# Kernel optimization log

Measured on AMD Instinct MI355X. Metric: run time of the kernel, lower is better.

The kernel has to match this reference:

```python
import jax, jax.numpy as jnp
import numpy as np

N_ENT = 200000   # n_entities
N_NODES = 20000  # nodes in subgraph
N_EDGES = 320000 # avg degree 16
R = 40           # n_relations
B = 34           # num_bases (hard-coded in module)
D_IN = 128       # emb_dim_init
D_HID = 128      # hidden_dim
D_OUT = 128      # out_dim


def setup_inputs() -> dict:
    key = jax.random.key(0)
    ks = jax.random.split(key, 14)
    s = 0.05
    return {
        "node_index": jax.random.randint(ks[0], (N_NODES,), 0, N_ENT),
        "edge_index": jax.random.randint(ks[1], (2, N_EDGES), 0, N_NODES),
        "edge_type": jax.random.randint(ks[2], (N_EDGES,), 0, R),
        "node_frequency": jax.random.normal(ks[3], (N_NODES,), jnp.float32),
        "node_emb": jax.random.normal(ks[4], (N_ENT, D_IN), jnp.float32),
        "comp0": jax.random.normal(ks[5], (R, B), jnp.float32) * s,
        "bases0": jax.random.normal(ks[6], (B, D_IN, D_HID), jnp.float32) * s,
        "root0": jax.random.normal(ks[7], (D_IN, D_HID), jnp.float32) * s,
        "bias0": jnp.zeros((D_HID,), jnp.float32),
        "comp1": jax.random.normal(ks[8], (R, B), jnp.float32) * s,
        "bases1": jax.random.normal(ks[9], (B, D_HID, D_OUT), jnp.float32) * s,
        "root1": jax.random.normal(ks[10], (D_HID, D_OUT), jnp.float32) * s,
        "bias1": jnp.zeros((D_OUT,), jnp.float32),
    }


def _rgcn_conv(x, src, dst, etype, comp, bases, root, bias):
    """Basis-decomposed RGCNConv (PyG semantics: per-relation mean aggregation
    over incoming edges, plus root transform and bias)."""
    n = x.shape[0]
    # relation weights from basis decomposition: [R, in, out]
    W = jnp.einsum('rb,bio->rio', comp, bases)
    # transform all nodes by every relation weight: [R, N, out]
    h_all = jnp.einsum('ni,rio->rno', x, W)
    # gather per-edge message x[src] @ W[edge_type]: [E, out]
    msg = h_all[etype, src]
    # mean-aggregate per (dst node, relation) segment
    seg = dst * R + etype
    sums = jax.ops.segment_sum(msg, seg, num_segments=n * R)  # [N*R, out]
    cnt = jax.ops.segment_sum(jnp.ones((msg.shape[0],), x.dtype), seg,
                              num_segments=n * R)
    mean = sums / jnp.maximum(cnt, 1.0)[:, None]
    agg = mean.reshape(n, R, -1).sum(axis=1)  # sum over relations: [N, out]
    return agg + x @ root + bias


def reference(node_index, edge_index, edge_type, node_frequency, node_emb,
              comp0, bases0, root0, bias0, comp1, bases1, root1, bias1):
    # node_frequency is accepted but unused (matches original forward).
    x = node_emb[node_index]                      # [N, D_IN]
    src, dst = edge_index[0], edge_index[1]
    x = _rgcn_conv(x, src, dst, edge_type, comp0, bases0, root0, bias0)
    x = _rgcn_conv(x, src, dst, edge_type, comp1, bases1, root1, bias1)
    return x
```

## Files before the change

kernel.cpp:

```cpp
#include <hip/hip_runtime.h>

#define N_NODES  20000
#define N_EDGES  320000
#define R_REL    40
#define N_BASES  34
#define DIM      128
#define EB       128
#define P_PAD    (N_EDGES + R_REL * EB)
#define ROOT_PAD ((N_NODES + EB - 1) / EB * EB)
#define P2_MAX   (P_PAD + ROOT_PAD)
#define NE2      (N_EDGES + N_NODES)
#define NSLOT    (R_REL + 1)
#define NBLK     (P2_MAX / EB)
#define PADW     (NSLOT * EB)

#define INIT_B   ((N_NODES * R_REL + 255) / 256)
#define GATH_B   (N_NODES * 16 / 256)
#define WT_B     (2 * NSLOT * 16)

typedef unsigned int uint;
typedef unsigned short ushort;
typedef __attribute__((ext_vector_type(8))) short short8;
typedef __attribute__((ext_vector_type(4))) float f32x4;

__device__ __forceinline__ ushort f2bf(float f) {
    uint u = __float_as_uint(f);
    return (ushort)((u + 0x7FFFu + ((u >> 16) & 1u)) >> 16);
}
__device__ __forceinline__ uint pk2bf(float a, float b) {
    return (uint)f2bf(a) | ((uint)f2bf(b) << 16);
}

__global__ void prep_kernel(int* __restrict__ c_cnt, int* __restrict__ meta_cur2_deg,
                            const float* __restrict__ emb, const int* __restrict__ idx,
                            ushort* __restrict__ xb,
                            const float* __restrict__ comp0, const float* __restrict__ bases0,
                            const float* __restrict__ root0,
                            const float* __restrict__ comp1, const float* __restrict__ bases1,
                            const float* __restrict__ root1,
                            ushort* __restrict__ Wt) {
    int b = blockIdx.x;
    int t = threadIdx.x;
    if (b < INIT_B) {
        int i = b * 256 + t;
        if (i < N_NODES * R_REL) c_cnt[i] = 0;
        if (i < 256 + 2 * N_NODES) meta_cur2_deg[i] = 0;
    } else if (b < INIT_B + GATH_B) {
        int g = (b - INIT_B) * 256 + t;
        int n = g >> 4, v = g & 15;
        const float4* s = (const float4*)(emb + (size_t)idx[n] * DIM + v * 8);
        float4 a = s[0], bb = s[1];
        uint4 o;
        o.x = pk2bf(a.x, a.y);  o.y = pk2bf(a.z, a.w);
        o.z = pk2bf(bb.x, bb.y); o.w = pk2bf(bb.z, bb.w);
        *(uint4*)(xb + (size_t)n * DIM + v * 8) = o;
    } else {
        __shared__ float tile[32][33];
        __shared__ float scomp[N_BASES];
        int wb = b - INIT_B - GATH_B;
        int layer = (wb >= NSLOT * 16) ? 1 : 0;
        int bb2 = wb - layer * NSLOT * 16;
        const float* comp  = layer ? comp1  : comp0;
        const float* bases = layer ? bases1 : bases0;
        const float* root  = layer ? root1  : root0;
        int slot = bb2 >> 4;
        int tb   = bb2 & 15;
        int k0 = (tb >> 2) * 32, n0 = (tb & 3) * 32;
        int tr = t >> 5, tc = t & 31;
        if (slot < R_REL) {
            if (t < N_BASES) scomp[t] = comp[slot * N_BASES + t];
            __syncthreads();
            #pragma unroll
            for (int i = 0; i < 4; ++i) {
                int kk = tr + 8 * i;
                float acc = 0.f;
                #pragma unroll
                for (int bs = 0; bs < N_BASES; ++bs)
                    acc += scomp[bs] * bases[((size_t)bs * DIM + k0 + kk) * DIM + n0 + tc];
                tile[kk][tc] = acc;
            }
        } else {
            #pragma unroll
            for (int i = 0; i < 4; ++i) {
                int kk = tr + 8 * i;
                tile[kk][tc] = root[(size_t)(k0 + kk) * DIM + n0 + tc];
            }
        }
        __syncthreads();
        size_t obase = ((size_t)layer * NSLOT + slot) * DIM * DIM;
        #pragma unroll
        for (int i = 0; i < 4; ++i) {
            int rr = tr + 8 * i;
            Wt[obase + (size_t)(n0 + rr) * DIM + k0 + tc] = f2bf(tile[tc][rr]);
        }
    }
}

__global__ void count_kernel(const int* __restrict__ ei, const int* __restrict__ et,
                             int* __restrict__ c, int* __restrict__ h,
                             int* __restrict__ deg) {
    __shared__ int hloc[R_REL];
    int t = threadIdx.x;
    if (t < R_REL) hloc[t] = 0;
    __syncthreads();
    int e = blockIdx.x * blockDim.x + t;
    if (e < N_EDGES) {
        int dst = ei[N_EDGES + e];
        int r   = et[e];
        atomicAdd(&c[dst * R_REL + r], 1);
        atomicAdd(&deg[dst], 1);
        atomicAdd(&hloc[r], 1);
    }
    __syncthreads();
    if (t < R_REL && hloc[t]) atomicAdd(&h[t], hloc[t]);
}

__global__ void scans_kernel(const int* __restrict__ deg, const int* __restrict__ h,
                             int* __restrict__ ptr, int* __restrict__ off,
                             int* __restrict__ brel) {
    __shared__ int part[1024];
    __shared__ int soff[R_REL + 2];
    const int CHn = (N_NODES + 1023) / 1024;
    int t = threadIdx.x;
    int s = 0;
    for (int i = 0; i < CHn; ++i) {
        int idx = t * CHn + i;
        if (idx < N_NODES) s += deg[idx] + 1;
    }
    part[t] = s;
    __syncthreads();
    for (int d = 1; d < 1024; d <<= 1) {
        int v = (t >= d) ? part[t - d] : 0;
        __syncthreads();
        part[t] += v;
        __syncthreads();
    }
    int base = (t > 0) ? part[t - 1] : 0;
    for (int i = 0; i < CHn; ++i) {
        int idx = t * CHn + i;
        if (idx < N_NODES) { ptr[idx] = base; base += deg[idx] + 1; }
    }
    if (t == 0) {
        ptr[N_NODES] = NE2;
        int acc = 0;
        soff[0] = 0; off[0] = 0;
        for (int r = 0; r < R_REL; ++r) {
            acc += ((h[r] + EB - 1) / EB) * EB;
            soff[r + 1] = acc; off[r + 1] = acc;
        }
        soff[R_REL + 1] = acc + ROOT_PAD;
        off[R_REL + 1]  = acc + ROOT_PAD;
    }
    __syncthreads();
    for (int i = t; i < NBLK; i += 1024) {
        int e0 = i * EB;
        int r = -1;
        if (e0 < soff[R_REL + 1]) {
            r = 0;
            while (e0 >= soff[r + 1]) ++r;
        }
        brel[i] = r;
    }
}

__global__ void place_kernel(const int* __restrict__ ei, const int* __restrict__ et,
                             const int* __restrict__ off, int* __restrict__ cur,
                             const int* __restrict__ c_cnt, const int* __restrict__ h,
                             const int* __restrict__ ptr, int* __restrict__ cur2,
                             uint4* __restrict__ esrc) {
    __shared__ int hloc[R_REL];
    __shared__ int base[R_REL];
    int t = threadIdx.x;
    if (t < R_REL) hloc[t] = 0;
    __syncthreads();
    int e = blockIdx.x * blockDim.x + t;
    int r = 0, myrank = 0, src = 0, dst = 0;
    bool isEdge = (e < N_EDGES);
    if (isEdge) {
        r = et[e]; src = ei[e]; dst = ei[N_EDGES + e];
        myrank = atomicAdd(&hloc[r], 1);
    }
    __syncthreads();
    if (t < R_REL) base[t] = hloc[t] ? atomicAdd(&cur[t], hloc[t]) : 0;
    __syncthreads();
    if (isEdge) {
        int p = off[r] + base[r] + myrank;
        int q = ptr[dst] + 1 + atomicAdd(&cur2[dst], 1);
        int cnt = c_cnt[dst * R_REL + r];
        float esc = 1.0f / (float)(cnt < 1 ? 1 : cnt);
        esrc[p] = make_uint4((uint)src, (uint)q, __float_as_uint(esc), 0u);
    } else if (e < NE2) {
        int n = e - N_EDGES;
        esrc[off[R_REL] + n] = make_uint4((uint)n, (uint)ptr[n], 0x3f800000u, 0u);
    } else if (e < NE2 + PADW) {
        int i = e - NE2;
        int pr = i >> 7, j = i & (EB - 1);
        int cnt = (pr < R_REL) ? h[pr] : N_NODES;
        int slot = off[pr] + cnt + j;
        if (slot < off[pr + 1])
            esrc[slot] = make_uint4((uint)-1, (uint)-1, 0u, 0u);
    }
}

__launch_bounds__(512)
__global__ void edge_mfma_kernel(const uint4* __restrict__ esrc, const int* __restrict__ brel,
                                 const ushort* __restrict__ xb, const ushort* __restrict__ Wt,
                                 ushort* __restrict__ T) {
    __shared__ __align__(16) ushort Ws[DIM * DIM];
    int r = brel[blockIdx.x];
    if (r < 0) return;
    int t = threadIdx.x;
    int e0 = blockIdx.x * EB;
    int wv = t >> 6;
    int l  = t & 63;
    int lr = l & 15;
    int lk = l >> 4;
    int er = e0 + wv * 16 + lr;
    uint4 es = esrc[er];

    const ushort* Wr = Wt + (size_t)r * DIM * DIM;
    #pragma unroll
    for (int i = 0; i < 4; ++i) {
        int idx = t + 512 * i;
        int row = idx >> 4, slot = idx & 15;
        uint4 v = *(const uint4*)(Wr + row * DIM + slot * 8);
        *(uint4*)(&Ws[row * DIM + ((slot ^ (row & 15)) * 8)]) = v;
    }

    int s0 = (int)es.x, q0 = (int)es.y;
    float esc = __uint_as_float(es.z);
    const ushort* xp = xb + (size_t)(s0 < 0 ? 0 : s0) * DIM;
    short8 xf[4];
    #pragma unroll
    for (int ks = 0; ks < 4; ++ks)
        xf[ks] = *(const short8*)(xp + (ks * 4 + lk) * 8);
    __syncthreads();

    f32x4 acc[8];
    #pragma unroll
    for (int mt = 0; mt < 8; ++mt) acc[mt] = (f32x4){0.f, 0.f, 0.f, 0.f};

    #pragma unroll
    for (int ks = 0; ks < 4; ++ks) {
        #pragma unroll
        for (int mt = 0; mt < 8; ++mt) {
            int row = mt * 16 + lr;
            int slot = (ks * 4 + lk) ^ lr;
            short8 wf = *(const short8*)(&Ws[row * DIM + slot * 8]);
            acc[mt] = __builtin_amdgcn_mfma_f32_16x16x32_bf16(wf, xf[ks], acc[mt], 0, 0, 0);
        }
    }

    if (q0 >= 0) {
        ushort* T0 = T + (size_t)q0 * DIM;
        #pragma unroll
        for (int mt = 0; mt < 8; ++mt) {
            uint2 p0;
            p0.x = pk2bf(acc[mt][0] * esc, acc[mt][1] * esc);
            p0.y = pk2bf(acc[mt][2] * esc, acc[mt][3] * esc);
            *(uint2*)(T0 + mt * 16 + lk * 4) = p0;
        }
    }
}

template<int OUT_BF16>
__global__ void aggregate_kernel(const int* __restrict__ ptr, const ushort* __restrict__ T,
                                 const float* __restrict__ bias, void* __restrict__ yout) {
    int t = threadIdx.x;
    int n = blockIdx.x * 2 + (t >> 6);
    int tt = t & 63;
    int s0 = ptr[n], s1 = ptr[n + 1];
    float a0 = bias[2 * tt], a1 = bias[2 * tt + 1];
    for (int q = s0; q < s1; ++q) {
        uint v = *(const uint*)(T + (size_t)q * DIM + 2 * tt);
        a0 += __uint_as_float(v << 16);
        a1 += __uint_as_float(v & 0xFFFF0000u);
    }
    if (OUT_BF16) {
        ((uint*)yout)[n * 64 + tt] = pk2bf(a0, a1);
    } else {
        ((float2*)yout)[n * 64 + tt] = make_float2(a0, a1);
    }
}

extern "C" void kernel_launch(void* const* d_in, const int* in_sizes, int n_in,
                              void* d_out, int out_size, void* d_ws, size_t ws_size,
                              hipStream_t stream) {
    const int*   node_index = (const int*)d_in[0];
    const int*   edge_index = (const int*)d_in[1];
    const int*   edge_type  = (const int*)d_in[2];
    const float* node_emb   = (const float*)d_in[4];
    const float* comp0  = (const float*)d_in[5];
    const float* bases0 = (const float*)d_in[6];
    const float* root0  = (const float*)d_in[7];
    const float* bias0  = (const float*)d_in[8];
    const float* comp1  = (const float*)d_in[9];
    const float* bases1 = (const float*)d_in[10];
    const float* root1  = (const float*)d_in[11];
    const float* bias1  = (const float*)d_in[12];
    float* out = (float*)d_out;

    char* ws = (char*)d_ws;
    int*    c_cnt  = (int*)   (ws);
    ushort* Wt     = (ushort*)(ws +  3200000);
    ushort* x0b    = (ushort*)(ws +  5886976);
    ushort* y0b    = (ushort*)(ws + 11006976);
    uint4*  esrc   = (uint4*) (ws + 16126976);
    int*    meta   = (int*)   (ws + 21650432);
    int*    cur2   = (int*)   (ws + 21651456);
    int*    deg    = (int*)   (ws + 21731456);
    int*    ptr    = (int*)   (ws + 21811456);
    int*    brel   = (int*)   (ws + 21891712);
    ushort* T      = (ushort*)(ws + 21904000);
    int* off = meta;
    int* h   = meta + 64;
    int* cur = meta + 128;

    prep_kernel<<<INIT_B + GATH_B + WT_B, 256, 0, stream>>>(
        c_cnt, meta, node_emb, node_index, x0b,
        comp0, bases0, root0, comp1, bases1, root1, Wt);
    count_kernel<<<(N_EDGES + 255) / 256, 256, 0, stream>>>(edge_index, edge_type, c_cnt, h, deg);
    scans_kernel<<<1, 1024, 0, stream>>>(deg, h, ptr, off, brel);
    place_kernel<<<(NE2 + PADW + 255) / 256, 256, 0, stream>>>(
        edge_index, edge_type, off, cur, c_cnt, h, ptr, cur2, esrc);

    edge_mfma_kernel<<<NBLK, 512, 0, stream>>>(esrc, brel, x0b, Wt, T);
    aggregate_kernel<1><<<N_NODES / 2, 128, 0, stream>>>(ptr, T, bias0, y0b);

    edge_mfma_kernel<<<NBLK, 512, 0, stream>>>(esrc, brel, y0b,
                                               Wt + (size_t)NSLOT * DIM * DIM, T);
    aggregate_kernel<0><<<N_NODES / 2, 128, 0, stream>>>(ptr, T, bias1, out);
}
```

Baseline: 255.4 us.

## Compute 20 relation weights per block reusing each loaded basis tile

The weight-construction blocks in the prep kernel now each compute 20 relations for one 32x32 tile, and each loaded basis element is reused across all 20 relations. Previously every relation re-read all 34 bases separately. Basis reads drop by about 20x, but the launch shrinks from 1312 weight blocks to 64 and each thread carries 80 accumulators, which lowers parallelism and raises register pressure.

```diff
diff --git a/kernel.cpp b/kernel.cpp
--- a/kernel.cpp
+++ b/kernel.cpp
@@ -16,7 +16,7 @@
 
 #define INIT_B   ((N_NODES * R_REL + 255) / 256)
 #define GATH_B   (N_NODES * 16 / 256)
-#define WT_B     (2 * NSLOT * 16)
+#define WT_B     64
 
 typedef unsigned int uint;
 typedef unsigned short ushort;
@@ -56,42 +56,63 @@
         *(uint4*)(xb + (size_t)n * DIM + v * 8) = o;
     } else {
         __shared__ float tile[32][33];
-        __shared__ float scomp[N_BASES];
+        __shared__ float scomp[20][N_BASES];
         int wb = b - INIT_B - GATH_B;
-        int layer = (wb >= NSLOT * 16) ? 1 : 0;
-        int bb2 = wb - layer * NSLOT * 16;
+        int layer = wb >> 5;
+        int chunk = (wb >> 4) & 1;
+        int tb    = wb & 15;
         const float* comp  = layer ? comp1  : comp0;
         const float* bases = layer ? bases1 : bases0;
         const float* root  = layer ? root1  : root0;
-        int slot = bb2 >> 4;
-        int tb   = bb2 & 15;
         int k0 = (tb >> 2) * 32, n0 = (tb & 3) * 32;
+        int cr0 = chunk * 20;
         int tr = t >> 5, tc = t & 31;
-        if (slot < R_REL) {
-            if (t < N_BASES) scomp[t] = comp[slot * N_BASES + t];
+        for (int i = t; i < 20 * N_BASES; i += 256)
+            scomp[i / N_BASES][i % N_BASES] = comp[(cr0 + i / N_BASES) * N_BASES + i % N_BASES];
+        __syncthreads();
+        float acc[20][4];
+        #pragma unroll
+        for (int r = 0; r < 20; ++r)
+            #pragma unroll
+            for (int i = 0; i < 4; ++i) acc[r][i] = 0.f;
+        for (int bs = 0; bs < N_BASES; ++bs) {
+            float t4[4];
+            #pragma unroll
+            for (int i = 0; i < 4; ++i)
+                t4[i] = bases[((size_t)bs * DIM + k0 + tr + 8 * i) * DIM + n0 + tc];
+            #pragma unroll
+            for (int r = 0; r < 20; ++r) {
+                float cv = scomp[r][bs];
+                #pragma unroll
+                for (int i = 0; i < 4; ++i) acc[r][i] += cv * t4[i];
+            }
+        }
+        size_t lbase = (size_t)layer * NSLOT * DIM * DIM;
+        #pragma unroll 1
+        for (int r = 0; r < 20; ++r) {
             __syncthreads();
             #pragma unroll
+            for (int i = 0; i < 4; ++i) tile[tr + 8 * i][tc] = acc[r][i];
+            __syncthreads();
+            size_t obase = lbase + (size_t)(cr0 + r) * DIM * DIM;
+            #pragma unroll
             for (int i = 0; i < 4; ++i) {
-                int kk = tr + 8 * i;
-                float acc = 0.f;
-                #pragma unroll
-                for (int bs = 0; bs < N_BASES; ++bs)
-                    acc += scomp[bs] * bases[((size_t)bs * DIM + k0 + kk) * DIM + n0 + tc];
-                tile[kk][tc] = acc;
+                int rr = tr + 8 * i;
+                Wt[obase + (size_t)(n0 + rr) * DIM + k0 + tc] = f2bf(tile[tc][rr]);
             }
-        } else {
+        }
+        if (chunk == 1) {
+            __syncthreads();
+            #pragma unroll
+            for (int i = 0; i < 4; ++i)
+                tile[tr + 8 * i][tc] = root[(size_t)(k0 + tr + 8 * i) * DIM + n0 + tc];
+            __syncthreads();
+            size_t obase = lbase + (size_t)R_REL * DIM * DIM;
             #pragma unroll
             for (int i = 0; i < 4; ++i) {
-                int kk = tr + 8 * i;
-                tile[kk][tc] = root[(size_t)(k0 + kk) * DIM + n0 + tc];
+                int rr = tr + 8 * i;
+                Wt[obase + (size_t)(n0 + rr) * DIM + k0 + tc] = f2bf(tile[tc][rr]);
             }
-        }
-        __syncthreads();
-        size_t obase = ((size_t)layer * NSLOT + slot) * DIM * DIM;
-        #pragma unroll
-        for (int i = 0; i < 4; ++i) {
-            int rr = tr + 8 * i;
-            Wt[obase + (size_t)(n0 + rr) * DIM + k0 + tc] = f2bf(tile[tc][rr]);
         }
     }
 }
```

New measurement: 286.5 us (median of 2 runs). +12.2%, slower.
